# Optimization experiments

Hardware: AMD Instinct MI355X
Metric: run time of the kernel (lower is better)

## Reference

```python
import jax, jax.numpy as jnp
import numpy as np

MAX_DELTAS = 4
PACK = 8  # 4-bit values packed into int32
HIDDEN = 4096
Q_SLICE = 4096   # num_heads(32) * head_size(128)
KV_SLICE = 1024  # num_kv_heads(8) * head_size(128)
TOKENS = 4096


def setup_inputs() -> dict:
    key = jax.random.key(0)
    ks = jax.random.split(key, 16)
    imax = 2**31 - 1
    inp = {
        "x": jax.random.normal(ks[0], (TOKENS, HIDDEN), dtype=jnp.float32),
        "base_weight": jax.random.normal(ks[1], (Q_SLICE + 2 * KV_SLICE, HIDDEN), dtype=jnp.float32) * 0.02,
        "qweight_q": jax.random.randint(ks[2], (MAX_DELTAS, 1, HIDDEN // PACK, Q_SLICE), 0, imax, dtype=jnp.int32),
        "qweight_k": jax.random.randint(ks[3], (MAX_DELTAS, 1, HIDDEN // PACK, KV_SLICE), 0, imax, dtype=jnp.int32),
        "qweight_v": jax.random.randint(ks[4], (MAX_DELTAS, 1, HIDDEN // PACK, KV_SLICE), 0, imax, dtype=jnp.int32),
        "qzeros_q": jax.random.randint(ks[5], (MAX_DELTAS, 1, 1, Q_SLICE // PACK), 0, imax, dtype=jnp.int32),
        "qzeros_k": jax.random.randint(ks[6], (MAX_DELTAS, 1, 1, KV_SLICE // PACK), 0, imax, dtype=jnp.int32),
        "qzeros_v": jax.random.randint(ks[7], (MAX_DELTAS, 1, 1, KV_SLICE // PACK), 0, imax, dtype=jnp.int32),
        "scales_q": jax.random.uniform(ks[8], (MAX_DELTAS, 1, 1, Q_SLICE), dtype=jnp.float32) * 0.01,
        "scales_k": jax.random.uniform(ks[9], (MAX_DELTAS, 1, 1, KV_SLICE), dtype=jnp.float32) * 0.01,
        "scales_v": jax.random.uniform(ks[10], (MAX_DELTAS, 1, 1, KV_SLICE), dtype=jnp.float32) * 0.01,
        "indices": jax.random.randint(ks[11], (TOKENS,), 0, MAX_DELTAS, dtype=jnp.int32),
    }
    return inp


def _unpack_rows(qw):
    # (D, 1, K//PACK, N) int32 -> (D, K, N) 4-bit values, packed along K
    D, _, Kp, N = qw.shape
    shifts = (jnp.arange(PACK, dtype=jnp.int32) * 4)
    q = (qw[:, 0, :, None, :] >> shifts[None, None, :, None]) & 0xF  # (D,Kp,PACK,N)
    return q.reshape(D, Kp * PACK, N)


def _unpack_cols(qz):
    # (D, 1, 1, N//PACK) int32 -> (D, N), packed along N
    D = qz.shape[0]
    shifts = (jnp.arange(PACK, dtype=jnp.int32) * 4)
    z = (qz[:, 0, 0, :, None] >> shifts[None, None, :]) & 0xF  # (D, N//PACK, PACK)
    return z.reshape(D, -1)


def _dequant(qw, qz, sc):
    # GPTQ-style dequant, single group (g_idx is all zeros): W = (q - (z+1)) * scale
    q = _unpack_rows(qw).astype(jnp.float32)            # (D, K, N)
    z = (_unpack_cols(qz) + 1).astype(jnp.float32)      # (D, N)
    return (q - z[:, None, :]) * sc[:, 0, 0, :][:, None, :]


def _delta_slice(x, indices, qw, qz, sc):
    # per-token indexed delta matmul: out[t] = x[t] @ W[indices[t]] (0 if index==-1)
    W = _dequant(qw, qz, sc)  # (D, K, N)
    out = jnp.zeros((x.shape[0], W.shape[2]), dtype=x.dtype)
    for d in range(MAX_DELTAS):
        mask = (indices == d).astype(x.dtype)[:, None]
        out = out + (x * mask) @ W[d]
    return out


def reference(x, base_weight, qweight_q, qweight_k, qweight_v,
              qzeros_q, qzeros_k, qzeros_v,
              scales_q, scales_k, scales_v, indices):
    # base merged QKV projection
    base_out = x @ base_weight.T  # (T, q + 2*kv)
    # per-slice delta adds (offsets handled by concatenation order: q, k, v)
    dq = _delta_slice(x, indices, qweight_q, qzeros_q, scales_q)
    dk = _delta_slice(x, indices, qweight_k, qzeros_k, scales_k)
    dv = _delta_slice(x, indices, qweight_v, qzeros_v, scales_v)
    return base_out + jnp.concatenate([dq, dk, dv], axis=1)
```

## Files before the change

### kernel.cpp

```cpp
#include <hip/hip_runtime.h>
#include <stdint.h>

#define TOKENS 4096
#define HIDDEN 4096
#define NQ     4096
#define NKV    1024
#define NTOT   6144
#define KPACK  512
#define MAXTILES 20

typedef __attribute__((ext_vector_type(8))) __bf16 bf16x8;
typedef __attribute__((ext_vector_type(8))) short short8v;
typedef __attribute__((ext_vector_type(4))) float floatx4;

__device__ __forceinline__ short f2bf(float f) {
  union { float f; unsigned u; } v; v.f = f;
  unsigned r = v.u + 0x7fffu + ((v.u >> 16) & 1u);
  return (short)(r >> 16);
}

__device__ __forceinline__ void load_lds16(const void* g, void* l) {
  __builtin_amdgcn_global_load_lds((__attribute__((address_space(1))) void*)(g),
                                   (__attribute__((address_space(3))) void*)(l),
                                   16, 0, 0);
}

#define VMCNT(n) asm volatile("s_waitcnt vmcnt(" #n ")" ::: "memory")

__global__ __launch_bounds__(256) void prep_tokens(const int* __restrict__ idx,
                                                   int* __restrict__ token_list,
                                                   int* __restrict__ grp) {
  __shared__ int cnt[4], cur[4];
  const int tid = threadIdx.x;
  if (tid < 4) cnt[tid] = 0;
  __syncthreads();
  for (int t = tid; t < TOKENS; t += 256) {
    int d = idx[t];
    if ((unsigned)d < 4u) atomicAdd(&cnt[d], 1);
  }
  __syncthreads();
  if (tid == 0) {
    int s = 0, nt = 0;
    for (int d = 0; d < 4; d++) {
      cur[d] = s; grp[d] = s; grp[4 + d] = cnt[d]; s += cnt[d];
      int tiles = (cnt[d] + 255) >> 8;
      for (int rt = 0; rt < tiles; rt++) grp[9 + nt++] = d | (rt << 2);
    }
    grp[8] = nt;
  }
  __syncthreads();
  for (int t = tid; t < TOKENS; t += 256) {
    int d = idx[t];
    if ((unsigned)d < 4u) {
      int p = atomicAdd(&cur[d], 1);
      token_list[p] = t;
    }
  }
}

__global__ __launch_bounds__(256) void cvt_x(const float* __restrict__ x,
                                             short* __restrict__ xb) {
  size_t g = (size_t)blockIdx.x * 256 + threadIdx.x;
  size_t i = g * 8;
  float4 a = ((const float4*)(x + i))[0];
  float4 b = ((const float4*)(x + i))[1];
  short8v o;
  o[0] = f2bf(a.x); o[1] = f2bf(a.y); o[2] = f2bf(a.z); o[3] = f2bf(a.w);
  o[4] = f2bf(b.x); o[5] = f2bf(b.y); o[6] = f2bf(b.z); o[7] = f2bf(b.w);
  *(short8v*)(xb + i) = o;
}

__global__ __launch_bounds__(256) void combine_w(
    const float* __restrict__ bw,
    const int* __restrict__ qwq, const int* __restrict__ qwk, const int* __restrict__ qwv,
    const int* __restrict__ qzq, const int* __restrict__ qzk, const int* __restrict__ qzv,
    const float* __restrict__ scq, const float* __restrict__ sck, const float* __restrict__ scv,
    short* __restrict__ wc) {
  __shared__ int ldsq[4][8][72];
  __shared__ float zs[4][64], ss[4][64];
  const int tid = threadIdx.x;
  const int n0  = blockIdx.y * 64;
  const int kp0 = blockIdx.x * 8;

  const int* qw; const int* qz; const float* sc; int Ns, nb;
  if (n0 < NQ)            { qw = qwq; qz = qzq; sc = scq; Ns = NQ;  nb = n0; }
  else if (n0 < NQ + NKV) { qw = qwk; qz = qzk; sc = sck; Ns = NKV; nb = n0 - NQ; }
  else                    { qw = qwv; qz = qzv; sc = scv; Ns = NKV; nb = n0 - NQ - NKV; }

  {
    int d = tid >> 6, n = tid & 63;
    int nn = nb + n;
    int z = (int)(((unsigned)qz[d * (Ns >> 3) + (nn >> 3)] >> ((nn & 7) * 4)) & 0xFu);
    zs[d][n] = (float)(z + 1);
    ss[d][n] = sc[d * Ns + nn];
  }

#pragma unroll
  for (int d = 0; d < 4; d++) {
#pragma unroll
    for (int p = 0; p < 2; p++) {
      int i  = tid + p * 256;
      int kp = i >> 6, n = i & 63;
      ldsq[d][kp][n] = qw[((size_t)d * KPACK + kp0 + kp) * Ns + nb + n];
    }
  }
  __syncthreads();

  const int kp = tid & 7;
#pragma unroll
  for (int p = 0; p < 2; p++) {
    int n = (tid >> 3) + p * 32;
    const float4* bp = (const float4*)(bw + (size_t)(n0 + n) * HIDDEN + (kp0 + kp) * 8);
    float4 b0 = bp[0], b1 = bp[1];
    float bv[8] = {b0.x, b0.y, b0.z, b0.w, b1.x, b1.y, b1.z, b1.w};
#pragma unroll
    for (int d = 0; d < 4; d++) {
      unsigned q32 = (unsigned)ldsq[d][kp][n];
      float z = zs[d][n], s = ss[d][n];
      short8v o;
#pragma unroll
      for (int j = 0; j < 8; j++)
        o[j] = f2bf(((float)((q32 >> (4 * j)) & 0xFu) - z) * s + bv[j]);
      *(short8v*)(wc + ((size_t)d * NTOT + n0 + n) * HIDDEN + (kp0 + kp) * 8) = o;
    }
  }
}

__device__ __forceinline__ void stage_t(int t, short* aBuf, short* bBuf,
                                        const short* gA0, const short* gA1,
                                        const short* gB0, const short* gB1,
                                        int wave) {
  const int ko = t * 32;
  short* la = aBuf + wave * 512;
  short* lb = bBuf + wave * 512;
  load_lds16(gA0 + ko, la);
  load_lds16(gA1 + ko, la + 4096);
  load_lds16(gB0 + ko, lb);
  load_lds16(gB1 + ko, lb + 4096);
}

__device__ __forceinline__ void compute_tile(const short* Ab, const short* Bb,
                                             int wm, int wn, int mrow, int sx,
                                             floatx4 acc[8][4]) {
  bf16x8 bfr[4], afr[4];
#pragma unroll
  for (int j = 0; j < 4; j++)
    bfr[j] = *(const bf16x8*)(Bb + (wn * 64 + j * 16 + mrow) * 32 + sx);
#pragma unroll
  for (int i = 0; i < 4; i++)
    afr[i] = *(const bf16x8*)(Ab + (wm * 128 + i * 16 + mrow) * 32 + sx);
  __builtin_amdgcn_s_setprio(1);
#pragma unroll
  for (int i = 0; i < 4; i++)
#pragma unroll
    for (int j = 0; j < 4; j++)
      acc[i][j] = __builtin_amdgcn_mfma_f32_16x16x32_bf16(afr[i], bfr[j], acc[i][j], 0, 0, 0);
  __builtin_amdgcn_s_setprio(0);
#pragma unroll
  for (int i = 0; i < 4; i++)
    afr[i] = *(const bf16x8*)(Ab + (wm * 128 + (i + 4) * 16 + mrow) * 32 + sx);
  __builtin_amdgcn_s_setprio(1);
#pragma unroll
  for (int i = 0; i < 4; i++)
#pragma unroll
    for (int j = 0; j < 4; j++)
      acc[i + 4][j] = __builtin_amdgcn_mfma_f32_16x16x32_bf16(afr[i], bfr[j], acc[i + 4][j], 0, 0, 0);
  __builtin_amdgcn_s_setprio(0);
}

#define GSTEP(CUR, NXT, TNXT, VM)                                     \
  stage_t(TNXT, &As[NXT][0], &Bs[NXT][0], gA0, gA1, gB0, gB1, wave);  \
  VMCNT(VM);                                                          \
  __builtin_amdgcn_s_barrier();                                       \
  __builtin_amdgcn_sched_barrier(0);                                  \
  compute_tile(&As[CUR][0], &Bs[CUR][0], wm, wn, mrow, sx, acc);

#define GSTEP_NOST(CUR, VM)                                           \
  VMCNT(VM);                                                          \
  __builtin_amdgcn_s_barrier();                                       \
  __builtin_amdgcn_sched_barrier(0);                                  \
  compute_tile(&As[CUR][0], &Bs[CUR][0], wm, wn, mrow, sx, acc);

__global__ __launch_bounds__(512, 2) void gemm_grouped(
    const short* __restrict__ xb, const short* __restrict__ wc,
    const int* __restrict__ token_list, const int* __restrict__ grp,
    float* __restrict__ out) {
  const int nt = grp[8];
  if ((int)blockIdx.y >= nt) return;
  const int te = grp[9 + blockIdx.y];
  const int d  = te & 3;
  const int rt = te >> 2;
  const int cnt   = grp[4 + d];
  const int start = grp[d];
  const int n0 = blockIdx.x * 256;

  __shared__ __align__(16) short As[4][8192];
  __shared__ __align__(16) short Bs[4][8192];
  __shared__ int toks[256];

  const int tid = threadIdx.x;
  if (tid < 256) {
    int r = rt * 256 + tid;
    if (r >= cnt) r = cnt - 1;
    toks[tid] = token_list[start + r];
  }
  __syncthreads();

  const int wave = tid >> 6;
  const int lane = tid & 63;

  const int sw = ((lane & 3) ^ ((lane >> 3) & 3)) * 8;

  const int arow = wave * 16 + (lane >> 2);
  const short* gA0 = xb + (size_t)toks[arow] * HIDDEN + sw;
  const short* gA1 = xb + (size_t)toks[arow + 128] * HIDDEN + sw;
  const short* wrow = wc + ((size_t)d * NTOT + n0) * HIDDEN;
  const short* gB0 = wrow + (size_t)arow * HIDDEN + sw;
  const short* gB1 = gB0 + (size_t)128 * HIDDEN;

  const int mrow = lane & 15;
  const int sx = (((lane >> 4) ^ ((mrow >> 1) & 3))) * 8;
  const int wm = wave >> 2;
  const int wn = wave & 3;

  floatx4 acc[8][4];
#pragma unroll
  for (int i = 0; i < 8; i++)
#pragma unroll
    for (int j = 0; j < 4; j++) acc[i][j] = (floatx4){0.f, 0.f, 0.f, 0.f};

  stage_t(0, &As[0][0], &Bs[0][0], gA0, gA1, gB0, gB1, wave);
  stage_t(1, &As[1][0], &Bs[1][0], gA0, gA1, gB0, gB1, wave);

  for (int it = 0; it < 31; ++it) {
    const int t = it * 4;
    GSTEP(0, 2, t + 2, 8);
    GSTEP(1, 3, t + 3, 8);
    GSTEP(2, 0, t + 4, 8);
    GSTEP(3, 1, t + 5, 8);
  }
  GSTEP(0, 2, 126, 8);
  GSTEP(1, 3, 127, 8);
  GSTEP_NOST(2, 4);
  GSTEP_NOST(3, 0);

  const int rbase = (lane >> 4) * 4;
  const int coll  = lane & 15;
#pragma unroll
  for (int i = 0; i < 8; i++) {
#pragma unroll
    for (int r = 0; r < 4; r++) {
      int m = wm * 128 + i * 16 + rbase + r;
      if (rt * 256 + m < cnt) {
        float* orow = out + (size_t)toks[m] * NTOT + n0 + wn * 64 + coll;
#pragma unroll
        for (int j = 0; j < 4; j++) orow[j * 16] = acc[i][j][r];
      }
    }
  }
}

extern "C" void kernel_launch(void* const* d_in, const int* in_sizes, int n_in,
                              void* d_out, int out_size, void* d_ws, size_t ws_size,
                              hipStream_t stream) {
  const float* x   = (const float*)d_in[0];
  const float* bw  = (const float*)d_in[1];
  const int*   qwq = (const int*)d_in[2];
  const int*   qwk = (const int*)d_in[3];
  const int*   qwv = (const int*)d_in[4];
  const int*   qzq = (const int*)d_in[5];
  const int*   qzk = (const int*)d_in[6];
  const int*   qzv = (const int*)d_in[7];
  const float* scq = (const float*)d_in[8];
  const float* sck = (const float*)d_in[9];
  const float* scv = (const float*)d_in[10];
  const int*   idx = (const int*)d_in[11];
  float* out = (float*)d_out;

  char* ws = (char*)d_ws;
  short* xb = (short*)ws;
  short* wc = (short*)(ws + (size_t)33554432);
  int* token_list = (int*)(ws + (size_t)33554432 + 201326592);
  int* grp = token_list + TOKENS;

  prep_tokens<<<1, 256, 0, stream>>>(idx, token_list, grp);
  cvt_x<<<(TOKENS * HIDDEN) / (256 * 8), 256, 0, stream>>>(x, xb);
  dim3 gc(HIDDEN / 64, NTOT / 64);
  combine_w<<<gc, 256, 0, stream>>>(bw, qwq, qwk, qwv, qzq, qzk, qzv, scq, sck, scv, wc);
  dim3 gg(NTOT / 256, MAXTILES);
  gemm_grouped<<<gg, 512, 0, stream>>>(xb, wc, token_list, grp, out);
}
```

Measured before the change: 570.3 us.

## Double-buffer LDS fragments in registers to overlap LDS reads with MFMA

Restructures the grouped GEMM main loop so the LDS fragment reads for the next k-tile are issued while the MFMAs for the current tile run from a second register fragment set. The global-to-LDS prefetch depth goes from two to three stages, with a reworked prologue and epilogue. The aim is to hide LDS read latency behind matrix math. The cost is a second set of 12 bf16x8 fragments per thread, which raises register pressure under launch_bounds(512,2) and could cause spills or lower occupancy.

```diff
diff --git a/kernel.cpp b/kernel.cpp
--- a/kernel.cpp
+++ b/kernel.cpp
@@ -24,8 +24,6 @@
                                    (__attribute__((address_space(3))) void*)(l),
                                    16, 0, 0);
 }
-
-#define VMCNT(n) asm volatile("s_waitcnt vmcnt(" #n ")" ::: "memory")
 
 __global__ __launch_bounds__(256) void prep_tokens(const int* __restrict__ idx,
                                                    int* __restrict__ token_list,
@@ -126,6 +124,8 @@
   }
 }
 
+struct Frags { bf16x8 a[8]; bf16x8 b[4]; };
+
 __device__ __forceinline__ void stage_t(int t, short* aBuf, short* bBuf,
                                         const short* gA0, const short* gA1,
                                         const short* gB0, const short* gB1,
@@ -139,47 +139,34 @@
   load_lds16(gB1 + ko, lb + 4096);
 }
 
-__device__ __forceinline__ void compute_tile(const short* Ab, const short* Bb,
-                                             int wm, int wn, int mrow, int sx,
-                                             floatx4 acc[8][4]) {
-  bf16x8 bfr[4], afr[4];
+__device__ __forceinline__ void lds_reads(const short* Ab, const short* Bb,
+                                          int wm, int wn, int mrow, int sx,
+                                          Frags& f) {
 #pragma unroll
   for (int j = 0; j < 4; j++)
-    bfr[j] = *(const bf16x8*)(Bb + (wn * 64 + j * 16 + mrow) * 32 + sx);
-#pragma unroll
-  for (int i = 0; i < 4; i++)
-    afr[i] = *(const bf16x8*)(Ab + (wm * 128 + i * 16 + mrow) * 32 + sx);
+    f.b[j] = *(const bf16x8*)(Bb + (wn * 64 + j * 16 + mrow) * 32 + sx);
+#pragma unroll
+  for (int i = 0; i < 8; i++)
+    f.a[i] = *(const bf16x8*)(Ab + (wm * 128 + i * 16 + mrow) * 32 + sx);
+}
+
+__device__ __forceinline__ void mfma_tile(const Frags& f, floatx4 acc[8][4]) {
   __builtin_amdgcn_s_setprio(1);
 #pragma unroll
-  for (int i = 0; i < 4; i++)
+  for (int i = 0; i < 8; i++)
 #pragma unroll
     for (int j = 0; j < 4; j++)
-      acc[i][j] = __builtin_amdgcn_mfma_f32_16x16x32_bf16(afr[i], bfr[j], acc[i][j], 0, 0, 0);
+      acc[i][j] = __builtin_amdgcn_mfma_f32_16x16x32_bf16(f.a[i], f.b[j], acc[i][j], 0, 0, 0);
   __builtin_amdgcn_s_setprio(0);
-#pragma unroll
-  for (int i = 0; i < 4; i++)
-    afr[i] = *(const bf16x8*)(Ab + (wm * 128 + (i + 4) * 16 + mrow) * 32 + sx);
-  __builtin_amdgcn_s_setprio(1);
-#pragma unroll
-  for (int i = 0; i < 4; i++)
-#pragma unroll
-    for (int j = 0; j < 4; j++)
-      acc[i + 4][j] = __builtin_amdgcn_mfma_f32_16x16x32_bf16(afr[i], bfr[j], acc[i + 4][j], 0, 0, 0);
-  __builtin_amdgcn_s_setprio(0);
-}
-
-#define GSTEP(CUR, NXT, TNXT, VM)                                     \
-  stage_t(TNXT, &As[NXT][0], &Bs[NXT][0], gA0, gA1, gB0, gB1, wave);  \
-  VMCNT(VM);                                                          \
-  __builtin_amdgcn_s_barrier();                                       \
-  __builtin_amdgcn_sched_barrier(0);                                  \
-  compute_tile(&As[CUR][0], &Bs[CUR][0], wm, wn, mrow, sx, acc);
-
-#define GSTEP_NOST(CUR, VM)                                           \
-  VMCNT(VM);                                                          \
-  __builtin_amdgcn_s_barrier();                                       \
-  __builtin_amdgcn_sched_barrier(0);                                  \
-  compute_tile(&As[CUR][0], &Bs[CUR][0], wm, wn, mrow, sx, acc);
+}
+
+#define GSTEP4(TNXT, SN, RN, FC, FN)                                        \
+  stage_t(TNXT, &As[SN][0], &Bs[SN][0], gA0, gA1, gB0, gB1, wave);          \
+  asm volatile("s_waitcnt vmcnt(8) lgkmcnt(0)" ::: "memory");               \
+  __builtin_amdgcn_s_barrier();                                             \
+  __builtin_amdgcn_sched_barrier(0);                                        \
+  lds_reads(&As[RN][0], &Bs[RN][0], wm, wn, mrow, sx, fr[FN]);              \
+  mfma_tile(fr[FC], acc);
 
 __global__ __launch_bounds__(512, 2) void gemm_grouped(
     const short* __restrict__ xb, const short* __restrict__ wc,
@@ -229,20 +216,35 @@
 #pragma unroll
     for (int j = 0; j < 4; j++) acc[i][j] = (floatx4){0.f, 0.f, 0.f, 0.f};
 
+  Frags fr[2];
+
   stage_t(0, &As[0][0], &Bs[0][0], gA0, gA1, gB0, gB1, wave);
   stage_t(1, &As[1][0], &Bs[1][0], gA0, gA1, gB0, gB1, wave);
+  stage_t(2, &As[2][0], &Bs[2][0], gA0, gA1, gB0, gB1, wave);
+  asm volatile("s_waitcnt vmcnt(8)" ::: "memory");
+  __builtin_amdgcn_s_barrier();
+  __builtin_amdgcn_sched_barrier(0);
+  lds_reads(&As[0][0], &Bs[0][0], wm, wn, mrow, sx, fr[0]);
 
   for (int it = 0; it < 31; ++it) {
     const int t = it * 4;
-    GSTEP(0, 2, t + 2, 8);
-    GSTEP(1, 3, t + 3, 8);
-    GSTEP(2, 0, t + 4, 8);
-    GSTEP(3, 1, t + 5, 8);
-  }
-  GSTEP(0, 2, 126, 8);
-  GSTEP(1, 3, 127, 8);
-  GSTEP_NOST(2, 4);
-  GSTEP_NOST(3, 0);
+    GSTEP4(t + 3, 3, 1, 0, 1);
+    GSTEP4(t + 4, 0, 2, 1, 0);
+    GSTEP4(t + 5, 1, 3, 0, 1);
+    GSTEP4(t + 6, 2, 0, 1, 0);
+  }
+  GSTEP4(127, 3, 1, 0, 1);
+  asm volatile("s_waitcnt vmcnt(4) lgkmcnt(0)" ::: "memory");
+  __builtin_amdgcn_s_barrier();
+  __builtin_amdgcn_sched_barrier(0);
+  lds_reads(&As[2][0], &Bs[2][0], wm, wn, mrow, sx, fr[0]);
+  mfma_tile(fr[1], acc);
+  asm volatile("s_waitcnt vmcnt(0) lgkmcnt(0)" ::: "memory");
+  __builtin_amdgcn_s_barrier();
+  __builtin_amdgcn_sched_barrier(0);
+  lds_reads(&As[3][0], &Bs[3][0], wm, wn, mrow, sx, fr[1]);
+  mfma_tile(fr[0], acc);
+  mfma_tile(fr[1], acc);
 
   const int rbase = (lane >> 4) * 4;
   const int coll  = lane & 15;
```

New measurement: 594.8 us. 1.04x slower.

## Restructure grouped GEMM main loop into 8-phase ping-pong schedule with split loads

Applied to the files above, without the earlier changes.

Replaces the 4-stage LDS ring with double-buffered 2x2 k-subtile buffers and an 8-phase loop. Each phase interleaves LDS fragment reads, one half of the next stage's global-to-LDS loads and a half-tile of MFMAs, with barriers on both sides. Row mapping per wave changes so each wave stages 32 contiguous rows. The aim is finer overlap of memory traffic with MFMA work in the style of HipKittens-like 8-wave ping-pong. The cost is more barriers per tile and tighter correctness constraints on vmcnt accounting.

```diff
diff --git a/kernel.cpp b/kernel.cpp
--- a/kernel.cpp
+++ b/kernel.cpp
@@ -24,8 +24,6 @@
                                    (__attribute__((address_space(3))) void*)(l),
                                    16, 0, 0);
 }
-
-#define VMCNT(n) asm volatile("s_waitcnt vmcnt(" #n ")" ::: "memory")
 
 __global__ __launch_bounds__(256) void prep_tokens(const int* __restrict__ idx,
                                                    int* __restrict__ token_list,
@@ -126,60 +124,49 @@
   }
 }
 
-__device__ __forceinline__ void stage_t(int t, short* aBuf, short* bBuf,
-                                        const short* gA0, const short* gA1,
-                                        const short* gB0, const short* gB1,
-                                        int wave) {
-  const int ko = t * 32;
-  short* la = aBuf + wave * 512;
-  short* lb = bBuf + wave * 512;
-  load_lds16(gA0 + ko, la);
-  load_lds16(gA1 + ko, la + 4096);
-  load_lds16(gB0 + ko, lb);
-  load_lds16(gB1 + ko, lb + 4096);
-}
-
-__device__ __forceinline__ void compute_tile(const short* Ab, const short* Bb,
-                                             int wm, int wn, int mrow, int sx,
-                                             floatx4 acc[8][4]) {
-  bf16x8 bfr[4], afr[4];
+__device__ __forceinline__ void rdB(const short* Bb, int wn, int mrow, int sx,
+                                    bf16x8 bf[4]) {
 #pragma unroll
   for (int j = 0; j < 4; j++)
-    bfr[j] = *(const bf16x8*)(Bb + (wn * 64 + j * 16 + mrow) * 32 + sx);
+    bf[j] = *(const bf16x8*)(Bb + (wn * 64 + j * 16 + mrow) * 32 + sx);
+}
+__device__ __forceinline__ void rdA(const short* Ab, int wm, int g, int mrow,
+                                    int sx, bf16x8 af[4]) {
 #pragma unroll
   for (int i = 0; i < 4; i++)
-    afr[i] = *(const bf16x8*)(Ab + (wm * 128 + i * 16 + mrow) * 32 + sx);
+    af[i] = *(const bf16x8*)(Ab + (wm * 128 + (g * 4 + i) * 16 + mrow) * 32 + sx);
+}
+__device__ __forceinline__ void mm(const bf16x8 af[4], const bf16x8 bf[4],
+                                   floatx4 acc[8][4], int g) {
   __builtin_amdgcn_s_setprio(1);
 #pragma unroll
   for (int i = 0; i < 4; i++)
 #pragma unroll
     for (int j = 0; j < 4; j++)
-      acc[i][j] = __builtin_amdgcn_mfma_f32_16x16x32_bf16(afr[i], bfr[j], acc[i][j], 0, 0, 0);
+      acc[g * 4 + i][j] =
+          __builtin_amdgcn_mfma_f32_16x16x32_bf16(af[i], bf[j], acc[g * 4 + i][j], 0, 0, 0);
   __builtin_amdgcn_s_setprio(0);
-#pragma unroll
-  for (int i = 0; i < 4; i++)
-    afr[i] = *(const bf16x8*)(Ab + (wm * 128 + (i + 4) * 16 + mrow) * 32 + sx);
-  __builtin_amdgcn_s_setprio(1);
-#pragma unroll
-  for (int i = 0; i < 4; i++)
-#pragma unroll
-    for (int j = 0; j < 4; j++)
-      acc[i + 4][j] = __builtin_amdgcn_mfma_f32_16x16x32_bf16(afr[i], bfr[j], acc[i + 4][j], 0, 0, 0);
-  __builtin_amdgcn_s_setprio(0);
-}
-
-#define GSTEP(CUR, NXT, TNXT, VM)                                     \
-  stage_t(TNXT, &As[NXT][0], &Bs[NXT][0], gA0, gA1, gB0, gB1, wave);  \
-  VMCNT(VM);                                                          \
-  __builtin_amdgcn_s_barrier();                                       \
-  __builtin_amdgcn_sched_barrier(0);                                  \
-  compute_tile(&As[CUR][0], &Bs[CUR][0], wm, wn, mrow, sx, acc);
-
-#define GSTEP_NOST(CUR, VM)                                           \
-  VMCNT(VM);                                                          \
-  __builtin_amdgcn_s_barrier();                                       \
-  __builtin_amdgcn_sched_barrier(0);                                  \
-  compute_tile(&As[CUR][0], &Bs[CUR][0], wm, wn, mrow, sx, acc);
+}
+__device__ __forceinline__ void st2(short* dst, const short* g0, const short* g1,
+                                    int ko) {
+  load_lds16(g0 + ko, dst);
+  load_lds16(g1 + ko, dst + 512);
+}
+
+#define BARRIER __builtin_amdgcn_s_barrier()
+#define LGKM0 asm volatile("s_waitcnt lgkmcnt(0)" ::: "memory")
+#define VMC4  asm volatile("s_waitcnt vmcnt(4)" ::: "memory")
+#define VMC0  asm volatile("s_waitcnt vmcnt(0)" ::: "memory")
+
+#define PH_O(RB, RA, SD, KO)                                   \
+  rdB(RB, wn, mrow, sx, bf);                                   \
+  rdA(RA, wm, 0, mrow, sx, af);                                \
+  st2((SD) + wave * 1024, gA0, gA1, (KO));                     \
+  BARRIER; LGKM0; mm(af, bf, acc, 0); BARRIER;
+#define PH_E(RA, SD, KO)                                       \
+  rdA(RA, wm, 1, mrow, sx, af);                                \
+  st2((SD) + wave * 1024, gB0, gB1, (KO));                     \
+  VMC4; BARRIER; LGKM0; mm(af, bf, acc, 1); BARRIER;
 
 __global__ __launch_bounds__(512, 2) void gemm_grouped(
     const short* __restrict__ xb, const short* __restrict__ wc,
@@ -194,8 +181,8 @@
   const int start = grp[d];
   const int n0 = blockIdx.x * 256;
 
-  __shared__ __align__(16) short As[4][8192];
-  __shared__ __align__(16) short Bs[4][8192];
+  __shared__ __align__(16) short Ak[2][2][8192];
+  __shared__ __align__(16) short Bk[2][2][8192];
   __shared__ int toks[256];
 
   const int tid = threadIdx.x;
@@ -211,12 +198,12 @@
 
   const int sw = ((lane & 3) ^ ((lane >> 3) & 3)) * 8;
 
-  const int arow = wave * 16 + (lane >> 2);
+  const int arow = wave * 32 + (lane >> 2);
   const short* gA0 = xb + (size_t)toks[arow] * HIDDEN + sw;
-  const short* gA1 = xb + (size_t)toks[arow + 128] * HIDDEN + sw;
+  const short* gA1 = xb + (size_t)toks[arow + 16] * HIDDEN + sw;
   const short* wrow = wc + ((size_t)d * NTOT + n0) * HIDDEN;
   const short* gB0 = wrow + (size_t)arow * HIDDEN + sw;
-  const short* gB1 = gB0 + (size_t)128 * HIDDEN;
+  const short* gB1 = gB0 + (size_t)16 * HIDDEN;
 
   const int mrow = lane & 15;
   const int sx = (((lane >> 4) ^ ((mrow >> 1) & 3))) * 8;
@@ -229,20 +216,40 @@
 #pragma unroll
     for (int j = 0; j < 4; j++) acc[i][j] = (floatx4){0.f, 0.f, 0.f, 0.f};
 
-  stage_t(0, &As[0][0], &Bs[0][0], gA0, gA1, gB0, gB1, wave);
-  stage_t(1, &As[1][0], &Bs[1][0], gA0, gA1, gB0, gB1, wave);
+  bf16x8 af[4], bf[4];
+
+  st2(&Ak[0][0][0] + wave * 1024, gA0, gA1, 0);
+  st2(&Bk[0][0][0] + wave * 1024, gB0, gB1, 0);
+  st2(&Ak[0][1][0] + wave * 1024, gA0, gA1, 32);
+  st2(&Bk[0][1][0] + wave * 1024, gB0, gB1, 32);
+  VMC4;
+  BARRIER;
 
   for (int it = 0; it < 31; ++it) {
-    const int t = it * 4;
-    GSTEP(0, 2, t + 2, 8);
-    GSTEP(1, 3, t + 3, 8);
-    GSTEP(2, 0, t + 4, 8);
-    GSTEP(3, 1, t + 5, 8);
-  }
-  GSTEP(0, 2, 126, 8);
-  GSTEP(1, 3, 127, 8);
-  GSTEP_NOST(2, 4);
-  GSTEP_NOST(3, 0);
+    const int kb = it * 128;
+    PH_O(&Bk[0][0][0], &Ak[0][0][0], &Ak[1][0][0], kb + 64);
+    PH_E(&Ak[0][0][0],               &Bk[1][0][0], kb + 64);
+    PH_O(&Bk[0][1][0], &Ak[0][1][0], &Ak[1][1][0], kb + 96);
+    PH_E(&Ak[0][1][0],               &Bk[1][1][0], kb + 96);
+    PH_O(&Bk[1][0][0], &Ak[1][0][0], &Ak[0][0][0], kb + 128);
+    PH_E(&Ak[1][0][0],               &Bk[0][0][0], kb + 128);
+    PH_O(&Bk[1][1][0], &Ak[1][1][0], &Ak[0][1][0], kb + 160);
+    PH_E(&Ak[1][1][0],               &Bk[0][1][0], kb + 160);
+  }
+  PH_O(&Bk[0][0][0], &Ak[0][0][0], &Ak[1][0][0], 4032);
+  PH_E(&Ak[0][0][0],               &Bk[1][0][0], 4032);
+  PH_O(&Bk[0][1][0], &Ak[0][1][0], &Ak[1][1][0], 4064);
+  PH_E(&Ak[0][1][0],               &Bk[1][1][0], 4064);
+  rdB(&Bk[1][0][0], wn, mrow, sx, bf);
+  rdA(&Ak[1][0][0], wm, 0, mrow, sx, af);
+  BARRIER; LGKM0; mm(af, bf, acc, 0); BARRIER;
+  rdA(&Ak[1][0][0], wm, 1, mrow, sx, af);
+  VMC0; BARRIER; LGKM0; mm(af, bf, acc, 1); BARRIER;
+  rdB(&Bk[1][1][0], wn, mrow, sx, bf);
+  rdA(&Ak[1][1][0], wm, 0, mrow, sx, af);
+  BARRIER; LGKM0; mm(af, bf, acc, 0); BARRIER;
+  rdA(&Ak[1][1][0], wm, 1, mrow, sx, af);
+  BARRIER; LGKM0; mm(af, bf, acc, 1);
 
   const int rbase = (lane >> 4) * 4;
   const int coll  = lane & 15;
```

New measurement: 572.1 us. Within noise of the previous version (+0.3%).
